# Performance work log

Measured on AMD Instinct MI355X. Metric: run time of the kernel, lower is better.

Reference implementation:

```python
import jax, jax.numpy as jnp
import numpy as np

N_EMBD = 16
HEAD_SIZE = 64
B, T = 8, 4096


def setup_inputs() -> dict:
    key = jax.random.key(0)
    k_x, k_q, k_k, k_v = jax.random.split(key, 4)
    # Uniform(0,1) keeps QK^T scores strictly positive so the fractional
    # power (-1/16) is well-defined (negative base would NaN, same as torch).
    x = jax.random.uniform(k_x, (B, T, N_EMBD), dtype=jnp.float32)
    Wq = jax.random.uniform(k_q, (N_EMBD, HEAD_SIZE), dtype=jnp.float32) * 0.25
    Wk = jax.random.uniform(k_k, (N_EMBD, HEAD_SIZE), dtype=jnp.float32) * 0.25
    Wv = jax.random.uniform(k_v, (N_EMBD, HEAD_SIZE), dtype=jnp.float32) * 0.25
    return {"x": x, "Wq": Wq, "Wk": Wk, "Wv": Wv}


def reference(x, Wq, Wk, Wv):
    features_dim = x.shape[-1]  # n_embd = 16
    q = x @ Wq                                   # [B, T, H]
    k = x @ Wk                                   # [B, T, H]
    scores = jnp.einsum('bth,bsh->bts', q, k)    # [B, T, T]
    scores = scores ** (-1.0 / features_dim)     # elementwise power, NOT a scale
    attn = jax.nn.softmax(scores, axis=1)        # softmax over QUERY axis (dim=1)
    v = x @ Wk                                   # faithful to source: uses keys_matrix, not Wv
    return jnp.einsum('bts,bsh->bth', attn, v)   # [B, T, H]
```

## Files before the change

kernel.cpp:

```cpp
#include <hip/hip_runtime.h>
#include <hip/hip_bf16.h>

#define BB 8
#define TT 4096
#define EE 16
#define HH 64
#define ZT 16
#define NS 8

typedef __attribute__((ext_vector_type(8))) __bf16 bf16x8;
typedef __attribute__((ext_vector_type(4))) __bf16 bf16x4;
typedef __attribute__((ext_vector_type(4))) float f32x4;

static __device__ __forceinline__ float exp_pow16(float d) {
    float L = __builtin_amdgcn_logf(d);
    float r = __builtin_fmaf(L, 2.72889e-6f, -1.536072e-4f);
    r = __builtin_fmaf(L, r, 4.946584e-3f);
    r = __builtin_fmaf(L, r, -0.11735442f);
    r = __builtin_fmaf(L, r, 2.71784054f);
    return r;
}

__global__ __launch_bounds__(256) void proj_kernel(
        const float* __restrict__ x, const float* __restrict__ Wq,
        const float* __restrict__ Wk,
        __bf16* __restrict__ Yb, __bf16* __restrict__ xb,
        float* __restrict__ Dsum) {
    __shared__ float Ms[16][16];
    __shared__ float xs[16][16];
    int tid = threadIdx.x;
    size_t gid = (size_t)blockIdx.x * 256 + tid;
    if (gid < (size_t)BB * TT / 4)
        ((float4*)Dsum)[gid] = (float4){0.f, 0.f, 0.f, 0.f};
    int i = tid >> 4, j = tid & 15;
    float m = 0.f;
#pragma unroll 8
    for (int h = 0; h < HH; ++h) m += Wq[i * HH + h] * Wk[j * HH + h];
    Ms[i][j] = m;
    int row0 = blockIdx.x * 16;
    xs[i][j] = x[(size_t)(row0 + i) * EE + j];
    __syncthreads();
    float y = 0.f;
#pragma unroll
    for (int k = 0; k < EE; ++k) y += xs[i][k] * Ms[k][j];
    size_t idx = (size_t)(row0 + i) * EE + j;
    Yb[idx] = (__bf16)y;
    xb[idx] = (__bf16)xs[i][j];
}

__global__ __launch_bounds__(256) void colsum_mfma(
        const __bf16* __restrict__ Yb, const __bf16* __restrict__ xb,
        float* __restrict__ Dsum) {
    int lane = threadIdx.x & 63;
    int w = threadIdx.x >> 6;
    int quad = lane >> 4;
    int l15 = lane & 15;
    int b = blockIdx.y;
    int z = blockIdx.z;
    int s0 = blockIdx.x * 256 + w * 64;

    const __bf16* xbb = xb + (size_t)b * TT * EE;
    const __bf16* Ybb = Yb + (size_t)b * TT * EE;

    bf16x8 bx[4];
#pragma unroll
    for (int st = 0; st < 4; ++st) {
        bf16x8 v = {};
        if (quad < 2)
            v = *(const bf16x8*)(xbb + (size_t)(s0 + st * 16 + l15) * EE + quad * 8);
        bx[st] = v;
    }

    const __bf16* gya = Ybb + (size_t)l15 * EE + (quad & 1) * 8;

    const int TL = TT / ZT;
    int t0 = z * TL, tend = t0 + TL;

    float csum[4] = {0.f, 0.f, 0.f, 0.f};

    auto LOADY = [&](bf16x8 ya[2], int t) {
#pragma unroll
        for (int ts = 0; ts < 2; ++ts)
            ya[ts] = *(const bf16x8*)(gya + (size_t)(t + ts * 16) * EE);
    };
    auto BODY = [&](bf16x8 ya[2]) {
#pragma unroll
        for (int st = 0; st < 4; ++st) {
#pragma unroll
            for (int ts = 0; ts < 2; ++ts) {
                f32x4 c = {0.f, 0.f, 0.f, 0.f};
                c = __builtin_amdgcn_mfma_f32_16x16x32_bf16(ya[ts], bx[st], c, 0, 0, 0);
                csum[st] += exp_pow16(c[0]) + exp_pow16(c[1])
                          + exp_pow16(c[2]) + exp_pow16(c[3]);
            }
        }
    };

    bf16x8 yaA[2], yaB[2];
    LOADY(yaA, t0);
    for (int t = t0; t < tend; t += 64) {
        LOADY(yaB, t + 32);
        BODY(yaA);
        int tn = (t + 64 < tend) ? (t + 64) : t0;
        LOADY(yaA, tn);
        BODY(yaB);
    }

#pragma unroll
    for (int st = 0; st < 4; ++st) {
        float r = csum[st];
        r += __shfl_xor(r, 16, 64);
        r += __shfl_xor(r, 32, 64);
        if (quad == 0)
            atomicAdd(&Dsum[(size_t)b * TT + s0 + st * 16 + l15], r);
    }
}

__global__ __launch_bounds__(256) void xd_kernel(
        const __bf16* __restrict__ xb, const float* __restrict__ Dsum,
        __bf16* __restrict__ xDT, float* __restrict__ Z) {
    __shared__ float Rs[64];
    __shared__ __bf16 tt[16][68];
    int b = blockIdx.y;
    int s0 = blockIdx.x * 64;
    int tid = threadIdx.x;
    size_t zi = ((size_t)b * gridDim.x + blockIdx.x) * 256 + tid;
    ((float4*)Z)[zi] = (float4){0.f, 0.f, 0.f, 0.f};
    if (tid < 64)
        Rs[tid] = 1.0f / Dsum[(size_t)b * TT + s0 + tid];
    __syncthreads();
    int sl = tid & 63, eg = tid >> 6;
    bf16x4 v = *(const bf16x4*)(xb + ((size_t)b * TT + s0 + sl) * EE + eg * 4);
    float r = Rs[sl];
#pragma unroll
    for (int i = 0; i < 4; ++i) tt[eg * 4 + i][sl] = (__bf16)((float)v[i] * r);
    __syncthreads();
    int e = tid >> 4, sc = tid & 15;
    *(bf16x4*)(xDT + ((size_t)b * EE + e) * TT + s0 + sc * 4) = *(const bf16x4*)&tt[e][sc * 4];
}

__global__ __launch_bounds__(256) void out_mfma(
        const __bf16* __restrict__ Yb, const __bf16* __restrict__ xb,
        const __bf16* __restrict__ xDT, float* __restrict__ Z) {
    __shared__ __bf16 Etile[2][4][2][16 * 40];

    int lane = threadIdx.x & 63;
    int w = threadIdx.x >> 6;
    int quad = lane >> 4;
    int l15 = lane & 15;
    int b = blockIdx.y;
    int z = blockIdx.z;
    int t0 = blockIdx.x * 128 + w * 32;

    const __bf16* xbb = xb + (size_t)b * TT * EE;
    const __bf16* Ybb = Yb + (size_t)b * TT * EE;
    const __bf16* xdb = xDT + (size_t)b * EE * TT;

    bf16x8 yf[2];
#pragma unroll
    for (int tile = 0; tile < 2; ++tile) {
        bf16x8 v = {};
        if (quad < 2)
            v = *(const bf16x8*)(Ybb + (size_t)(t0 + tile * 16 + l15) * EE + quad * 8);
        yf[tile] = v;
    }

    f32x4 acc[2] = {{0.f, 0.f, 0.f, 0.f}, {0.f, 0.f, 0.f, 0.f}};

    const __bf16* gaf = xbb + (size_t)l15 * EE + (quad & 1) * 8;
    const __bf16* gxd = xdb + (size_t)l15 * TT + quad * 8;

    const int SL = TT / NS;
    int s0z = z * SL, send = s0z + SL;

    auto LOADF = [&](bf16x8 af[2], bf16x8& bxd, int s) {
#pragma unroll
        for (int ss = 0; ss < 2; ++ss)
            af[ss] = *(const bf16x8*)(gaf + (size_t)(s + ss * 16) * EE);
        bxd = *(const bf16x8*)(gxd + s);
    };
    auto STAGE = [&](bf16x8 af[2], int p) {
#pragma unroll
        for (int tile = 0; tile < 2; ++tile) {
#pragma unroll
            for (int ss = 0; ss < 2; ++ss) {
                f32x4 c = {0.f, 0.f, 0.f, 0.f};
                c = __builtin_amdgcn_mfma_f32_16x16x32_bf16(af[ss], yf[tile], c, 0, 0, 0);
                bf16x4 e;
#pragma unroll
                for (int r = 0; r < 4; ++r)
                    e[r] = (__bf16)exp_pow16(c[r]);
                *(bf16x4*)&Etile[p][w][tile][l15 * 40 + ss * 16 + quad * 4] = e;
            }
        }
    };
    auto PV = [&](bf16x8& bxd, int p) {
#pragma unroll
        for (int tile = 0; tile < 2; ++tile) {
            bf16x8 aE = *(const bf16x8*)&Etile[p][w][tile][l15 * 40 + quad * 8];
            acc[tile] = __builtin_amdgcn_mfma_f32_16x16x32_bf16(aE, bxd, acc[tile], 0, 0, 0);
        }
    };

    bf16x8 afA[2], afB[2], bxdA, bxdB;
    LOADF(afA, bxdA, s0z);
    STAGE(afA, 0);
    for (int s = s0z; s < send; s += 64) {
        LOADF(afB, bxdB, s + 32);
        STAGE(afB, 1);
        PV(bxdA, 0);
        int sn = s + 64;
        if (sn < send) {
            LOADF(afA, bxdA, sn);
            STAGE(afA, 0);
        }
        PV(bxdB, 1);
    }

    float* zp = Z + ((size_t)b * TT + t0) * EE;
#pragma unroll
    for (int tile = 0; tile < 2; ++tile)
#pragma unroll
        for (int r = 0; r < 4; ++r)
            atomicAdd(&zp[(size_t)(tile * 16 + quad * 4 + r) * EE + l15], acc[tile][r]);
}

__global__ __launch_bounds__(256) void zout_kernel(
        const float* __restrict__ Z, const float* __restrict__ Wk,
        float* __restrict__ out) {
    __shared__ float zs[64][16];
    int b = blockIdx.y;
    int t0 = blockIdx.x * 64;
    int tid = threadIdx.x;
    ((float4*)zs)[tid] = ((const float4*)(Z + ((size_t)b * TT + t0) * EE))[tid];
    __syncthreads();
    int h = tid & 63, tg = tid >> 6;
    float wcol[16];
#pragma unroll
    for (int e = 0; e < EE; ++e) wcol[e] = Wk[e * HH + h];
    float* ob = out + ((size_t)b * TT + t0) * HH + h;
#pragma unroll
    for (int k = 0; k < 16; ++k) {
        int tl = tg * 16 + k;
        float o = 0.f;
#pragma unroll
        for (int e = 0; e < EE; ++e) o = __builtin_fmaf(zs[tl][e], wcol[e], o);
        ob[(size_t)tl * HH] = o;
    }
}

extern "C" void kernel_launch(void* const* d_in, const int* in_sizes, int n_in,
                              void* d_out, int out_size, void* d_ws, size_t ws_size,
                              hipStream_t stream) {
    const float* x  = (const float*)d_in[0];
    const float* Wq = (const float*)d_in[1];
    const float* Wk = (const float*)d_in[2];

    const size_t NE16 = (size_t)BB * TT * EE;
    char* wp = (char*)d_ws;
    __bf16* Yb   = (__bf16*)wp;  wp += NE16 * 2;
    __bf16* xbb  = (__bf16*)wp;  wp += NE16 * 2;
    __bf16* xDT  = (__bf16*)wp;  wp += NE16 * 2;
    float*  Dsum = (float*)wp;   wp += (size_t)BB * TT * 4;
    float*  Zws  = (float*)wp;

    float* out = (float*)d_out;

    proj_kernel<<<BB * TT / 16, 256, 0, stream>>>(x, Wq, Wk, Yb, xbb, Dsum);
    colsum_mfma<<<dim3(TT / 256, BB, ZT), 256, 0, stream>>>(Yb, xbb, Dsum);
    xd_kernel<<<dim3(TT / 64, BB), 256, 0, stream>>>(xbb, Dsum, xDT, Zws);
    out_mfma<<<dim3(TT / 128, BB, NS), 256, 0, stream>>>(Yb, xbb, xDT, Zws);
    zout_kernel<<<dim3(TT / 64, BB), 256, 0, stream>>>(Zws, Wk, out);
}
```

Measured before the change: 146.2 us.

## Fuse normalize and output stages into preceding kernels via last-block counters

Removes two kernel launches. The column-normalization/transpose step moves into the tail of colsum_mfma, and the Z·Wk output projection moves into the tail of out_mfma. Each uses an atomic arrival counter so only the last split block does the finishing work. Z and counter zeroing move into proj_kernel. The exp polynomial's constant term is folded out of the inner loop and added once per column, saving one FMA per element. This adds threadfence/atomic overhead, serial tail work in a single block per tile, and uncoalesced strided xDT stores.

Result: slower. 381.7 us (+161.2%).

```diff
diff --git a/kernel.cpp b/kernel.cpp
--- a/kernel.cpp
+++ b/kernel.cpp
@@ -25,13 +25,18 @@
         const float* __restrict__ x, const float* __restrict__ Wq,
         const float* __restrict__ Wk,
         __bf16* __restrict__ Yb, __bf16* __restrict__ xb,
-        float* __restrict__ Dsum) {
+        float* __restrict__ Dsum, float* __restrict__ Z,
+        int* __restrict__ cnt) {
     __shared__ float Ms[16][16];
     __shared__ float xs[16][16];
     int tid = threadIdx.x;
     size_t gid = (size_t)blockIdx.x * 256 + tid;
     if (gid < (size_t)BB * TT / 4)
         ((float4*)Dsum)[gid] = (float4){0.f, 0.f, 0.f, 0.f};
+    if (gid < (size_t)BB * TT * EE / 4)
+        ((float4*)Z)[gid] = (float4){0.f, 0.f, 0.f, 0.f};
+    if (blockIdx.x == 0)
+        for (int i = tid; i < 384; i += 256) cnt[i] = 0;
     int i = tid >> 4, j = tid & 15;
     float m = 0.f;
 #pragma unroll 8
@@ -50,7 +55,9 @@
 
 __global__ __launch_bounds__(256) void colsum_mfma(
         const __bf16* __restrict__ Yb, const __bf16* __restrict__ xb,
-        float* __restrict__ Dsum) {
+        float* __restrict__ Dsum, __bf16* __restrict__ xDT,
+        int* __restrict__ cnt1) {
+    __shared__ int isLast;
     int lane = threadIdx.x & 63;
     int w = threadIdx.x >> 6;
     int quad = lane >> 4;
@@ -90,8 +97,14 @@
             for (int ts = 0; ts < 2; ++ts) {
                 f32x4 c = {0.f, 0.f, 0.f, 0.f};
                 c = __builtin_amdgcn_mfma_f32_16x16x32_bf16(ya[ts], bx[st], c, 0, 0, 0);
-                csum[st] += exp_pow16(c[0]) + exp_pow16(c[1])
-                          + exp_pow16(c[2]) + exp_pow16(c[3]);
+#pragma unroll
+                for (int r = 0; r < 4; ++r) {
+                    float L = __builtin_amdgcn_logf(c[r]);
+                    float p = __builtin_fmaf(L, 2.72889e-6f, -1.536072e-4f);
+                    p = __builtin_fmaf(L, p, 4.946584e-3f);
+                    p = __builtin_fmaf(L, p, -0.11735442f);
+                    csum[st] = __builtin_fmaf(L, p, csum[st]);
+                }
             }
         }
     };
@@ -112,37 +125,42 @@
         r += __shfl_xor(r, 16, 64);
         r += __shfl_xor(r, 32, 64);
         if (quad == 0)
-            atomicAdd(&Dsum[(size_t)b * TT + s0 + st * 16 + l15], r);
-    }
-}
-
-__global__ __launch_bounds__(256) void xd_kernel(
-        const __bf16* __restrict__ xb, const float* __restrict__ Dsum,
-        __bf16* __restrict__ xDT, float* __restrict__ Z) {
-    __shared__ float Rs[64];
-    __shared__ __bf16 tt[16][68];
-    int b = blockIdx.y;
-    int s0 = blockIdx.x * 64;
+            atomicAdd(&Dsum[(size_t)b * TT + s0 + st * 16 + l15],
+                      r + 256.0f * 2.71784054f);
+    }
+
+    __syncthreads();
+    __threadfence();
+    if (threadIdx.x == 0) {
+        int old = atomicAdd(&cnt1[b * (TT / 256) + blockIdx.x], 1);
+        isLast = (old == ZT - 1);
+    }
+    __syncthreads();
+    if (!isLast) return;
+
     int tid = threadIdx.x;
-    size_t zi = ((size_t)b * gridDim.x + blockIdx.x) * 256 + tid;
-    ((float4*)Z)[zi] = (float4){0.f, 0.f, 0.f, 0.f};
-    if (tid < 64)
-        Rs[tid] = 1.0f / Dsum[(size_t)b * TT + s0 + tid];
-    __syncthreads();
-    int sl = tid & 63, eg = tid >> 6;
-    bf16x4 v = *(const bf16x4*)(xb + ((size_t)b * TT + s0 + sl) * EE + eg * 4);
-    float r = Rs[sl];
-#pragma unroll
-    for (int i = 0; i < 4; ++i) tt[eg * 4 + i][sl] = (__bf16)((float)v[i] * r);
-    __syncthreads();
-    int e = tid >> 4, sc = tid & 15;
-    *(bf16x4*)(xDT + ((size_t)b * EE + e) * TT + s0 + sc * 4) = *(const bf16x4*)&tt[e][sc * 4];
+    int s = blockIdx.x * 256 + tid;
+    float d = atomicAdd(&Dsum[(size_t)b * TT + s], 0.0f);
+    float rv = 1.0f / d;
+    const __bf16* xr = xbb + (size_t)s * EE;
+    bf16x8 x0 = *(const bf16x8*)xr;
+    bf16x8 x1 = *(const bf16x8*)(xr + 8);
+    __bf16* xdp = xDT + (size_t)b * EE * TT + s;
+#pragma unroll
+    for (int e = 0; e < 8; ++e)
+        xdp[(size_t)e * TT] = (__bf16)((float)x0[e] * rv);
+#pragma unroll
+    for (int e = 0; e < 8; ++e)
+        xdp[(size_t)(e + 8) * TT] = (__bf16)((float)x1[e] * rv);
 }
 
 __global__ __launch_bounds__(256) void out_mfma(
         const __bf16* __restrict__ Yb, const __bf16* __restrict__ xb,
-        const __bf16* __restrict__ xDT, float* __restrict__ Z) {
+        const __bf16* __restrict__ xDT, float* __restrict__ Z,
+        const float* __restrict__ Wk, float* __restrict__ out,
+        int* __restrict__ cnt2) {
     __shared__ __bf16 Etile[2][4][2][16 * 40];
+    __shared__ int isLast;
 
     int lane = threadIdx.x & 63;
     int w = threadIdx.x >> 6;
@@ -223,28 +241,36 @@
 #pragma unroll
         for (int r = 0; r < 4; ++r)
             atomicAdd(&zp[(size_t)(tile * 16 + quad * 4 + r) * EE + l15], acc[tile][r]);
-}
-
-__global__ __launch_bounds__(256) void zout_kernel(
-        const float* __restrict__ Z, const float* __restrict__ Wk,
-        float* __restrict__ out) {
-    __shared__ float zs[64][16];
-    int b = blockIdx.y;
-    int t0 = blockIdx.x * 64;
+
+    __syncthreads();
+    __threadfence();
+    if (threadIdx.x == 0) {
+        int old = atomicAdd(&cnt2[b * (TT / 128) + blockIdx.x], 1);
+        isLast = (old == NS - 1);
+    }
+    __syncthreads();
+    if (!isLast) return;
+
     int tid = threadIdx.x;
-    ((float4*)zs)[tid] = ((const float4*)(Z + ((size_t)b * TT + t0) * EE))[tid];
+    int t0b = blockIdx.x * 128;
+    float* zs = (float*)&Etile[0][0][0][0];
+    float* Zbase = Z + ((size_t)b * TT + t0b) * EE;
+#pragma unroll
+    for (int i = tid; i < 128 * 16; i += 256)
+        zs[i] = atomicAdd(&Zbase[i], 0.0f);
     __syncthreads();
     int h = tid & 63, tg = tid >> 6;
     float wcol[16];
 #pragma unroll
     for (int e = 0; e < EE; ++e) wcol[e] = Wk[e * HH + h];
-    float* ob = out + ((size_t)b * TT + t0) * HH + h;
-#pragma unroll
-    for (int k = 0; k < 16; ++k) {
-        int tl = tg * 16 + k;
+    float* ob = out + ((size_t)b * TT + t0b) * HH + h;
+#pragma unroll
+    for (int k = 0; k < 32; ++k) {
+        int tl = tg * 32 + k;
         float o = 0.f;
 #pragma unroll
-        for (int e = 0; e < EE; ++e) o = __builtin_fmaf(zs[tl][e], wcol[e], o);
+        for (int e = 0; e < EE; ++e)
+            o = __builtin_fmaf(zs[tl * 16 + e], wcol[e], o);
         ob[(size_t)tl * HH] = o;
     }
 }
@@ -262,13 +288,14 @@
     __bf16* xbb  = (__bf16*)wp;  wp += NE16 * 2;
     __bf16* xDT  = (__bf16*)wp;  wp += NE16 * 2;
     float*  Dsum = (float*)wp;   wp += (size_t)BB * TT * 4;
-    float*  Zws  = (float*)wp;
+    float*  Zws  = (float*)wp;   wp += NE16 * 4;
+    int*    cnt  = (int*)wp;
+    int*    cnt1 = cnt;
+    int*    cnt2 = cnt + 128;
 
     float* out = (float*)d_out;
 
-    proj_kernel<<<BB * TT / 16, 256, 0, stream>>>(x, Wq, Wk, Yb, xbb, Dsum);
-    colsum_mfma<<<dim3(TT / 256, BB, ZT), 256, 0, stream>>>(Yb, xbb, Dsum);
-    xd_kernel<<<dim3(TT / 64, BB), 256, 0, stream>>>(xbb, Dsum, xDT, Zws);
-    out_mfma<<<dim3(TT / 128, BB, NS), 256, 0, stream>>>(Yb, xbb, xDT, Zws);
-    zout_kernel<<<dim3(TT / 64, BB), 256, 0, stream>>>(Zws, Wk, out);
-}
+    proj_kernel<<<BB * TT / 16, 256, 0, stream>>>(x, Wq, Wk, Yb, xbb, Dsum, Zws, cnt);
+    colsum_mfma<<<dim3(TT / 256, BB, ZT), 256, 0, stream>>>(Yb, xbb, Dsum, xDT, cnt1);
+    out_mfma<<<dim3(TT / 128, BB, NS), 256, 0, stream>>>(Yb, xbb, xDT, Zws, Wk, out, cnt2);
+}
```

## Switch score MFMAs to 32x32x16 bf16 and hoist constant exp term

Applied to the files above, without the earlier changes.

Both score kernels now use 32x32x16 bf16 MFMA tiles instead of 16x16x32 tiles with half the lanes zero-padded for the K=16 dimension, so no MFMA work is wasted on padding. The Etile LDS layout is reorganized to match the 32x32 output layout. In colsum, the constant term of the exp polynomial is dropped from the inner loop and added once per column as 256 times the constant, saving one add per element. The change risks different LDS bank-conflict behaviour and register pressure from the 16-wide accumulators.

After: 141.4 us. 1.03x faster.

```diff
diff --git a/kernel.cpp b/kernel.cpp
--- a/kernel.cpp
+++ b/kernel.cpp
@@ -11,6 +11,7 @@
 typedef __attribute__((ext_vector_type(8))) __bf16 bf16x8;
 typedef __attribute__((ext_vector_type(4))) __bf16 bf16x4;
 typedef __attribute__((ext_vector_type(4))) float f32x4;
+typedef __attribute__((ext_vector_type(16))) float f32x16;
 
 static __device__ __forceinline__ float exp_pow16(float d) {
     float L = __builtin_amdgcn_logf(d);
@@ -53,8 +54,8 @@
         float* __restrict__ Dsum) {
     int lane = threadIdx.x & 63;
     int w = threadIdx.x >> 6;
-    int quad = lane >> 4;
-    int l15 = lane & 15;
+    int wl = lane & 31;
+    int hi = lane >> 5;
     int b = blockIdx.y;
     int z = blockIdx.z;
     int s0 = blockIdx.x * 256 + w * 64;
@@ -62,57 +63,51 @@
     const __bf16* xbb = xb + (size_t)b * TT * EE;
     const __bf16* Ybb = Yb + (size_t)b * TT * EE;
 
-    bf16x8 bx[4];
-#pragma unroll
-    for (int st = 0; st < 4; ++st) {
-        bf16x8 v = {};
-        if (quad < 2)
-            v = *(const bf16x8*)(xbb + (size_t)(s0 + st * 16 + l15) * EE + quad * 8);
-        bx[st] = v;
-    }
-
-    const __bf16* gya = Ybb + (size_t)l15 * EE + (quad & 1) * 8;
+    bf16x8 bx[2];
+#pragma unroll
+    for (int sg = 0; sg < 2; ++sg)
+        bx[sg] = *(const bf16x8*)(xbb + (size_t)(s0 + sg * 32 + wl) * EE + hi * 8);
+
+    const __bf16* gya = Ybb + (size_t)wl * EE + hi * 8;
 
     const int TL = TT / ZT;
     int t0 = z * TL, tend = t0 + TL;
 
-    float csum[4] = {0.f, 0.f, 0.f, 0.f};
-
-    auto LOADY = [&](bf16x8 ya[2], int t) {
-#pragma unroll
-        for (int ts = 0; ts < 2; ++ts)
-            ya[ts] = *(const bf16x8*)(gya + (size_t)(t + ts * 16) * EE);
+    float csum[2] = {0.f, 0.f};
+
+    auto BODY = [&](bf16x8 ya) {
+#pragma unroll
+        for (int sg = 0; sg < 2; ++sg) {
+            f32x16 c = {};
+            c = __builtin_amdgcn_mfma_f32_32x32x16_bf16(ya, bx[sg], c, 0, 0, 0);
+#pragma unroll
+            for (int r = 0; r < 16; ++r) {
+                float L = __builtin_amdgcn_logf(c[r]);
+                float p = __builtin_fmaf(L, 2.72889e-6f, -1.536072e-4f);
+                p = __builtin_fmaf(L, p, 4.946584e-3f);
+                p = __builtin_fmaf(L, p, -0.11735442f);
+                csum[sg] = __builtin_fmaf(L, p, csum[sg]);
+            }
+        }
     };
-    auto BODY = [&](bf16x8 ya[2]) {
-#pragma unroll
-        for (int st = 0; st < 4; ++st) {
-#pragma unroll
-            for (int ts = 0; ts < 2; ++ts) {
-                f32x4 c = {0.f, 0.f, 0.f, 0.f};
-                c = __builtin_amdgcn_mfma_f32_16x16x32_bf16(ya[ts], bx[st], c, 0, 0, 0);
-                csum[st] += exp_pow16(c[0]) + exp_pow16(c[1])
-                          + exp_pow16(c[2]) + exp_pow16(c[3]);
-            }
-        }
-    };
-
-    bf16x8 yaA[2], yaB[2];
-    LOADY(yaA, t0);
+
+    bf16x8 yaA, yaB;
+    yaA = *(const bf16x8*)(gya + (size_t)t0 * EE);
     for (int t = t0; t < tend; t += 64) {
-        LOADY(yaB, t + 32);
+        yaB = *(const bf16x8*)(gya + (size_t)(t + 32) * EE);
         BODY(yaA);
         int tn = (t + 64 < tend) ? (t + 64) : t0;
-        LOADY(yaA, tn);
+        yaA = *(const bf16x8*)(gya + (size_t)tn * EE);
         BODY(yaB);
     }
 
 #pragma unroll
-    for (int st = 0; st < 4; ++st) {
-        float r = csum[st];
-        r += __shfl_xor(r, 16, 64);
+    for (int sg = 0; sg < 2; ++sg) {
+        float r = csum[sg];
         r += __shfl_xor(r, 32, 64);
-        if (quad == 0)
-            atomicAdd(&Dsum[(size_t)b * TT + s0 + st * 16 + l15], r);
+        if (lane < 32)
+            atomicAdd(&Dsum[(size_t)b * TT + s0 + sg * 32 + wl],
+                      r + 256.0f * 2.71784054f);
     }
 }
 
@@ -142,10 +137,12 @@
 __global__ __launch_bounds__(256) void out_mfma(
         const __bf16* __restrict__ Yb, const __bf16* __restrict__ xb,
         const __bf16* __restrict__ xDT, float* __restrict__ Z) {
-    __shared__ __bf16 Etile[2][4][2][16 * 40];
+    __shared__ __bf16 Etile[2][4][32 * 36];
 
     int lane = threadIdx.x & 63;
     int w = threadIdx.x >> 6;
+    int wl = lane & 31;
+    int hi = lane >> 5;
     int quad = lane >> 4;
     int l15 = lane & 15;
     int b = blockIdx.y;
@@ -156,62 +153,49 @@
     const __bf16* Ybb = Yb + (size_t)b * TT * EE;
     const __bf16* xdb = xDT + (size_t)b * EE * TT;
 
-    bf16x8 yf[2];
-#pragma unroll
-    for (int tile = 0; tile < 2; ++tile) {
-        bf16x8 v = {};
-        if (quad < 2)
-            v = *(const bf16x8*)(Ybb + (size_t)(t0 + tile * 16 + l15) * EE + quad * 8);
-        yf[tile] = v;
-    }
+    bf16x8 yf = *(const bf16x8*)(Ybb + (size_t)(t0 + wl) * EE + hi * 8);
 
     f32x4 acc[2] = {{0.f, 0.f, 0.f, 0.f}, {0.f, 0.f, 0.f, 0.f}};
 
-    const __bf16* gaf = xbb + (size_t)l15 * EE + (quad & 1) * 8;
+    const __bf16* gaf = xbb + (size_t)wl * EE + hi * 8;
     const __bf16* gxd = xdb + (size_t)l15 * TT + quad * 8;
 
     const int SL = TT / NS;
     int s0z = z * SL, send = s0z + SL;
 
-    auto LOADF = [&](bf16x8 af[2], bf16x8& bxd, int s) {
-#pragma unroll
-        for (int ss = 0; ss < 2; ++ss)
-            af[ss] = *(const bf16x8*)(gaf + (size_t)(s + ss * 16) * EE);
-        bxd = *(const bf16x8*)(gxd + s);
-    };
-    auto STAGE = [&](bf16x8 af[2], int p) {
-#pragma unroll
-        for (int tile = 0; tile < 2; ++tile) {
-#pragma unroll
-            for (int ss = 0; ss < 2; ++ss) {
-                f32x4 c = {0.f, 0.f, 0.f, 0.f};
-                c = __builtin_amdgcn_mfma_f32_16x16x32_bf16(af[ss], yf[tile], c, 0, 0, 0);
-                bf16x4 e;
-#pragma unroll
-                for (int r = 0; r < 4; ++r)
-                    e[r] = (__bf16)exp_pow16(c[r]);
-                *(bf16x4*)&Etile[p][w][tile][l15 * 40 + ss * 16 + quad * 4] = e;
-            }
+    auto STAGE = [&](bf16x8 af, int p) {
+        f32x16 c = {};
+        c = __builtin_amdgcn_mfma_f32_32x32x16_bf16(af, yf, c, 0, 0, 0);
+#pragma unroll
+        for (int g = 0; g < 4; ++g) {
+            bf16x4 e;
+#pragma unroll
+            for (int r = 0; r < 4; ++r)
+                e[r] = (__bf16)exp_pow16(c[g * 4 + r]);
+            *(bf16x4*)&Etile[p][w][wl * 36 + g * 8 + hi * 4] = e;
         }
     };
     auto PV = [&](bf16x8& bxd, int p) {
 #pragma unroll
-        for (int tile = 0; tile < 2; ++tile) {
-            bf16x8 aE = *(const bf16x8*)&Etile[p][w][tile][l15 * 40 + quad * 8];
-            acc[tile] = __builtin_amdgcn_mfma_f32_16x16x32_bf16(aE, bxd, acc[tile], 0, 0, 0);
+        for (int h2 = 0; h2 < 2; ++h2) {
+            bf16x8 aE = *(const bf16x8*)&Etile[p][w][(h2 * 16 + l15) * 36 + quad * 8];
+            acc[h2] = __builtin_amdgcn_mfma_f32_16x16x32_bf16(aE, bxd, acc[h2], 0, 0, 0);
         }
     };
 
-    bf16x8 afA[2], afB[2], bxdA, bxdB;
-    LOADF(afA, bxdA, s0z);
+    bf16x8 afA, afB, bxdA, bxdB;
+    afA = *(const bf16x8*)(gaf + (size_t)s0z * EE);
+    bxdA = *(const bf16x8*)(gxd + s0z);
     STAGE(afA, 0);
     for (int s = s0z; s < send; s += 64) {
-        LOADF(afB, bxdB, s + 32);
+        afB = *(const bf16x8*)(gaf + (size_t)(s + 32) * EE);
+        bxdB = *(const bf16x8*)(gxd + (s + 32));
         STAGE(afB, 1);
         PV(bxdA, 0);
         int sn = s + 64;
         if (sn < send) {
-            LOADF(afA, bxdA, sn);
+            afA = *(const bf16x8*)(gaf + (size_t)sn * EE);
+            bxdA = *(const bf16x8*)(gxd + sn);
             STAGE(afA, 0);
         }
         PV(bxdB, 1);
@@ -219,10 +203,10 @@
 
     float* zp = Z + ((size_t)b * TT + t0) * EE;
 #pragma unroll
-    for (int tile = 0; tile < 2; ++tile)
+    for (int h2 = 0; h2 < 2; ++h2)
 #pragma unroll
         for (int r = 0; r < 4; ++r)
-            atomicAdd(&zp[(size_t)(tile * 16 + quad * 4 + r) * EE + l15], acc[tile][r]);
+            atomicAdd(&zp[(size_t)(h2 * 16 + quad * 4 + r) * EE + l15], acc[h2][r]);
 }
 
 __global__ __launch_bounds__(256) void zout_kernel(
```
